# Optimization experiments

Hardware: AMD Instinct MI355X
Metric: run time of the kernel (lower is better)

## Reference

```python
import jax, jax.numpy as jnp
import numpy as np

B, S, H, NH = 2, 2048, 1024, 16
HD = H // NH

def setup_inputs() -> dict:
    key = jax.random.key(0)
    ks = jax.random.split(key, 10)
    f = lambda k, shape, scale: jax.random.normal(k, shape, dtype=jnp.float32) * scale
    return {
        "hidden_states": f(ks[0], (B, S, H), 1.0),
        "attention_mask": f(ks[1], (B, 1, S, S), 1.0),
        # static weights: randn * static_ratio(0.9); dynamic: randn * 0.01
        "q_static": f(ks[2], (H, H), 0.9), "q_dynamic": f(ks[3], (H, H), 0.01),
        "k_static": f(ks[4], (H, H), 0.9), "k_dynamic": f(ks[5], (H, H), 0.01),
        "v_static": f(ks[6], (H, H), 0.9), "v_dynamic": f(ks[7], (H, H), 0.01),
        "o_static": f(ks[8], (H, H), 0.9), "o_dynamic": f(ks[9], (H, H), 0.01),
    }

def _split_heads(x):
    # [B, S, H] -> [B, NH, S, HD]
    b, s, _ = x.shape
    return x.reshape(b, s, NH, HD).transpose(0, 2, 1, 3)

def reference(hidden_states, attention_mask,
              q_static, q_dynamic, k_static, k_dynamic,
              v_static, v_dynamic, o_static, o_dynamic):
    # DualWeightLinear: y = x @ (static + dynamic)^T  (no bias)
    q = hidden_states @ (q_static + q_dynamic).T
    k = hidden_states @ (k_static + k_dynamic).T
    v = hidden_states @ (v_static + v_dynamic).T
    q, k, v = _split_heads(q), _split_heads(k), _split_heads(v)  # [B,NH,S,HD]
    scale = 1.0 / np.sqrt(HD).astype(np.float32)
    scores = jnp.einsum('bhqd,bhkd->bhqk', q, k) * scale  # [B,NH,S,S]
    scores = scores + attention_mask  # additive mask, broadcast over heads
    attn = jax.nn.softmax(scores, axis=-1)
    out = jnp.einsum('bhqk,bhkd->bhqd', attn, v)
    out = out.transpose(0, 2, 1, 3).reshape(hidden_states.shape[0], hidden_states.shape[1], H)
    return out @ (o_static + o_dynamic).T
```

## Files before the change

### kernel.cpp

```cpp
#include <hip/hip_runtime.h>
#include <hip/hip_bf16.h>
#include <stdint.h>

#define BB 2
#define SS 2048
#define HH 1024
#define NHH 16
#define HDD 64
#define MM (BB*SS)

typedef __attribute__((ext_vector_type(8))) short short8;
typedef __attribute__((ext_vector_type(4))) float f32x4;
typedef __attribute__((ext_vector_type(4))) unsigned short u16x4;

__device__ __forceinline__ unsigned short f2bf(float x){
  unsigned u = __float_as_uint(x);
  u += 0x7fffu + ((u >> 16) & 1u);
  return (unsigned short)(u >> 16);
}
__device__ __forceinline__ float bf2f(unsigned short h){
  return __uint_as_float(((unsigned)h) << 16);
}

__global__ void k_split(const float* __restrict__ in, unsigned short* __restrict__ hi,
                        unsigned short* __restrict__ lo, int n4){
  int i = blockIdx.x * blockDim.x + threadIdx.x;
  if (i >= n4) return;
  f32x4 x = ((const f32x4*)in)[i];
  u16x4 h, l;
  #pragma unroll
  for (int j = 0; j < 4; ++j){
    unsigned short hb = f2bf(x[j]);
    h[j] = hb;
    l[j] = f2bf(x[j] - bf2f(hb));
  }
  ((u16x4*)hi)[i] = h;
  ((u16x4*)lo)[i] = l;
}

__global__ void k_addsplit(const float* __restrict__ a, const float* __restrict__ b,
                           unsigned short* __restrict__ hi, unsigned short* __restrict__ lo, int n4){
  int i = blockIdx.x * blockDim.x + threadIdx.x;
  if (i >= n4) return;
  f32x4 x = ((const f32x4*)a)[i] + ((const f32x4*)b)[i];
  u16x4 h, l;
  #pragma unroll
  for (int j = 0; j < 4; ++j){
    unsigned short hb = f2bf(x[j]);
    h[j] = hb;
    l[j] = f2bf(x[j] - bf2f(hb));
  }
  ((u16x4*)hi)[i] = h;
  ((u16x4*)lo)[i] = l;
}

__global__ void k_addplain(const float* __restrict__ a, const float* __restrict__ b,
                           unsigned short* __restrict__ w, int n4){
  int i = blockIdx.x * blockDim.x + threadIdx.x;
  if (i >= n4) return;
  f32x4 x = ((const f32x4*)a)[i] + ((const f32x4*)b)[i];
  u16x4 h;
  #pragma unroll
  for (int j = 0; j < 4; ++j) h[j] = f2bf(x[j]);
  ((u16x4*)w)[i] = h;
}

template<int EPI>
__global__ __launch_bounds__(256, 2)
void gemm_bt(const unsigned short* __restrict__ A, const unsigned short* __restrict__ Bm,
             void* __restrict__ Cout, int M, int N, int K)
{
  __shared__ unsigned short As[128*32];
  __shared__ unsigned short Bs[128*32];
  const int tid = threadIdx.x;
  const int mb0 = blockIdx.y * 128, nb0 = blockIdx.x * 128;
  const int w  = tid >> 6, lane = tid & 63;
  const int wr = w >> 1,  wc = w & 1;
  const int lg = lane >> 4, lr = lane & 15;

  f32x4 zero4 = {0.f, 0.f, 0.f, 0.f};
  f32x4 acc[4][4];
  #pragma unroll
  for (int mi = 0; mi < 4; ++mi)
    #pragma unroll
    for (int ni = 0; ni < 4; ++ni) acc[mi][ni] = zero4;

  const unsigned short* Abase = A  + (size_t)mb0 * K;
  const unsigned short* Bbase = Bm + (size_t)nb0 * K;

  for (int kb = 0; kb < K; kb += 32) {
    __syncthreads();
    #pragma unroll
    for (int i = 0; i < 2; ++i){
      int c = i*256 + tid;
      int row = c >> 2, off = (c & 3) << 3;
      size_t go = (size_t)row * K + kb + off;
      __builtin_amdgcn_global_load_lds(
          (const __attribute__((address_space(1))) void*)(Abase + go),
          (__attribute__((address_space(3))) void*)(&As[c*8]), 16, 0, 0);
      __builtin_amdgcn_global_load_lds(
          (const __attribute__((address_space(1))) void*)(Bbase + go),
          (__attribute__((address_space(3))) void*)(&Bs[c*8]), 16, 0, 0);
    }
    __syncthreads();
    short8 af[4], bfr[4];
    #pragma unroll
    for (int mi = 0; mi < 4; ++mi) af[mi]  = *(const short8*)&As[(wr*64 + mi*16 + lr)*32 + lg*8];
    #pragma unroll
    for (int ni = 0; ni < 4; ++ni) bfr[ni] = *(const short8*)&Bs[(wc*64 + ni*16 + lr)*32 + lg*8];
    #pragma unroll
    for (int mi = 0; mi < 4; ++mi)
      #pragma unroll
      for (int ni = 0; ni < 4; ++ni)
        acc[mi][ni] = __builtin_amdgcn_mfma_f32_16x16x32_bf16(af[mi], bfr[ni], acc[mi][ni], 0, 0, 0);
  }

  #pragma unroll
  for (int mi = 0; mi < 4; ++mi){
    #pragma unroll
    for (int ni = 0; ni < 4; ++ni){
      int n  = nb0 + wc*64 + ni*16 + lr;
      int m0 = mb0 + wr*64 + mi*16 + 4*lg;
      if constexpr (EPI == 1) {
        unsigned short* vt = (unsigned short*)Cout;
        int b = m0 >> 11, s0 = m0 & 2047;
        u16x4 pk;
        #pragma unroll
        for (int r = 0; r < 4; ++r) pk[r] = f2bf(acc[mi][ni][r]);
        *(u16x4*)&vt[((size_t)(b*HH + n))*SS + s0] = pk;
      } else {
        float* C = (float*)Cout;
        #pragma unroll
        for (int r = 0; r < 4; ++r) C[(size_t)(m0 + r)*N + n] = acc[mi][ni][r];
      }
    }
  }
}

__global__ __launch_bounds__(256, 2)
void gemm_bt_split(const unsigned short* __restrict__ Ah, const unsigned short* __restrict__ Al,
                   const unsigned short* __restrict__ Bh, const unsigned short* __restrict__ Bl,
                   unsigned short* __restrict__ Ch, unsigned short* __restrict__ Cl,
                   int M, int N, int K)
{
  __shared__ unsigned short Ash[128*32], Asl[128*32], Bsh[128*32], Bsl[128*32];
  const int tid = threadIdx.x;
  const int mb0 = blockIdx.y * 128, nb0 = blockIdx.x * 128;
  const int w  = tid >> 6, lane = tid & 63;
  const int wr = w >> 1,  wc = w & 1;
  const int lg = lane >> 4, lr = lane & 15;

  f32x4 zero4 = {0.f, 0.f, 0.f, 0.f};
  f32x4 acc[4][4];
  #pragma unroll
  for (int mi = 0; mi < 4; ++mi)
    #pragma unroll
    for (int ni = 0; ni < 4; ++ni) acc[mi][ni] = zero4;

  const unsigned short* Ahb = Ah + (size_t)mb0 * K;
  const unsigned short* Alb = Al + (size_t)mb0 * K;
  const unsigned short* Bhb = Bh + (size_t)nb0 * K;
  const unsigned short* Blb = Bl + (size_t)nb0 * K;

  for (int kb = 0; kb < K; kb += 32) {
    __syncthreads();
    #pragma unroll
    for (int i = 0; i < 2; ++i){
      int c = i*256 + tid;
      int row = c >> 2, off = (c & 3) << 3;
      size_t go = (size_t)row * K + kb + off;
      __builtin_amdgcn_global_load_lds(
          (const __attribute__((address_space(1))) void*)(Ahb + go),
          (__attribute__((address_space(3))) void*)(&Ash[c*8]), 16, 0, 0);
      __builtin_amdgcn_global_load_lds(
          (const __attribute__((address_space(1))) void*)(Alb + go),
          (__attribute__((address_space(3))) void*)(&Asl[c*8]), 16, 0, 0);
      __builtin_amdgcn_global_load_lds(
          (const __attribute__((address_space(1))) void*)(Bhb + go),
          (__attribute__((address_space(3))) void*)(&Bsh[c*8]), 16, 0, 0);
      __builtin_amdgcn_global_load_lds(
          (const __attribute__((address_space(1))) void*)(Blb + go),
          (__attribute__((address_space(3))) void*)(&Bsl[c*8]), 16, 0, 0);
    }
    __syncthreads();
    short8 ah4[4], al4[4], bh4[4], bl4[4];
    #pragma unroll
    for (int mi = 0; mi < 4; ++mi){
      int ro = (wr*64 + mi*16 + lr)*32 + lg*8;
      ah4[mi] = *(const short8*)&Ash[ro];
      al4[mi] = *(const short8*)&Asl[ro];
    }
    #pragma unroll
    for (int ni = 0; ni < 4; ++ni){
      int ro = (wc*64 + ni*16 + lr)*32 + lg*8;
      bh4[ni] = *(const short8*)&Bsh[ro];
      bl4[ni] = *(const short8*)&Bsl[ro];
    }
    #pragma unroll
    for (int mi = 0; mi < 4; ++mi)
      #pragma unroll
      for (int ni = 0; ni < 4; ++ni){
        acc[mi][ni] = __builtin_amdgcn_mfma_f32_16x16x32_bf16(ah4[mi], bh4[ni], acc[mi][ni], 0, 0, 0);
        acc[mi][ni] = __builtin_amdgcn_mfma_f32_16x16x32_bf16(al4[mi], bh4[ni], acc[mi][ni], 0, 0, 0);
        acc[mi][ni] = __builtin_amdgcn_mfma_f32_16x16x32_bf16(ah4[mi], bl4[ni], acc[mi][ni], 0, 0, 0);
      }
  }

  #pragma unroll
  for (int mi = 0; mi < 4; ++mi){
    #pragma unroll
    for (int ni = 0; ni < 4; ++ni){
      int n  = nb0 + wc*64 + ni*16 + lr;
      int m0 = mb0 + wr*64 + mi*16 + 4*lg;
      #pragma unroll
      for (int r = 0; r < 4; ++r){
        float x = acc[mi][ni][r];
        unsigned short hb = f2bf(x);
        unsigned short lb = f2bf(x - bf2f(hb));
        size_t o = (size_t)(m0 + r)*N + n;
        Ch[o] = hb;
        Cl[o] = lb;
      }
    }
  }
}

__global__ __launch_bounds__(512, 4)
void attn_fwd(const unsigned short* __restrict__ qh, const unsigned short* __restrict__ ql,
              const unsigned short* __restrict__ kh, const unsigned short* __restrict__ kl,
              const unsigned short* __restrict__ vt, const float* __restrict__ mask,
              unsigned short* __restrict__ ao)
{
  __shared__ unsigned short Ksh[2][64*64];
  __shared__ unsigned short Ksl[2][64*64];
  __shared__ unsigned short Vss[2][64*64];
  __shared__ unsigned short P[8][16*64];

  const int tid = threadIdx.x;
  const int w = tid >> 6, lane = tid & 63;
  const int lg = lane >> 4, lr = lane & 15;
  const int xork = (lr & 7) << 4;

  const int bid = (blockIdx.x & 7) * 64 + (blockIdx.x >> 3);
  const int qb = bid & 15, h = (bid >> 4) & 15, b = bid >> 8;
  const int q0 = qb*128 + w*16;
  const int hoff = h*64;

  const int srow = tid >> 3;
  const int sgx  = (tid & 7) ^ (srow & 7);

  short8 qfh[2], qfl[2];
  {
    size_t qoff = ((size_t)(b*SS + q0 + lr))*HH + hoff + lg*8;
    qfh[0] = *(const short8*)(qh + qoff);
    qfl[0] = *(const short8*)(ql + qoff);
    qfh[1] = *(const short8*)(qh + qoff + 32);
    qfl[1] = *(const short8*)(ql + qoff + 32);
  }

  float m_run[4] = {-1e30f, -1e30f, -1e30f, -1e30f};
  float l_run[4] = {0.f, 0.f, 0.f, 0.f};
  f32x4 zero4 = {0.f, 0.f, 0.f, 0.f};
  f32x4 acc[4];
  #pragma unroll
  for (int d4 = 0; d4 < 4; ++d4) acc[d4] = zero4;
  const size_t mrow = ((size_t)(b*SS + q0 + 4*lg))*SS;

  #define ATTN_STAGE(buf, kvb) do {                                              \
    size_t kro = ((size_t)(b*SS + (kvb) + srow))*HH + hoff + sgx*8;              \
    size_t vro = ((size_t)(b*HH + hoff + srow))*SS + (kvb) + sgx*8;              \
    __builtin_amdgcn_global_load_lds(                                            \
        (const __attribute__((address_space(1))) void*)(kh + kro),               \
        (__attribute__((address_space(3))) void*)(&Ksh[buf][tid*8]), 16, 0, 0);  \
    __builtin_amdgcn_global_load_lds(                                            \
        (const __attribute__((address_space(1))) void*)(kl + kro),               \
        (__attribute__((address_space(3))) void*)(&Ksl[buf][tid*8]), 16, 0, 0);  \
    __builtin_amdgcn_global_load_lds(                                            \
        (const __attribute__((address_space(1))) void*)(vt + vro),               \
        (__attribute__((address_space(3))) void*)(&Vss[buf][tid*8]), 16, 0, 0);  \
  } while (0)

  ATTN_STAGE(0, 0);

  for (int t = 0; t < SS/64; ++t) {
    const int kv = t*64;
    const int cur = t & 1;
    __syncthreads();
    if (t + 1 < SS/64) ATTN_STAGE(cur ^ 1, kv + 64);

    float mk[4][4];
    #pragma unroll
    for (int r = 0; r < 4; ++r)
      #pragma unroll
      for (int nb = 0; nb < 4; ++nb)
        mk[r][nb] = mask[mrow + (size_t)r*SS + kv + nb*16 + lr];

    f32x4 sc[4];
    #pragma unroll
    for (int nb = 0; nb < 4; ++nb) {
      const int krow = (nb*16 + lr)*64;
      const int c0 = ((0   + lg*16) ^ xork) >> 1;
      const int c1 = ((64  + lg*16) ^ xork) >> 1;
      short8 k0h = *(const short8*)&Ksh[cur][krow + c0];
      short8 k1h = *(const short8*)&Ksh[cur][krow + c1];
      short8 k0l = *(const short8*)&Ksl[cur][krow + c0];
      short8 k1l = *(const short8*)&Ksl[cur][krow + c1];
      f32x4 d = zero4;
      d = __builtin_amdgcn_mfma_f32_16x16x32_bf16(qfh[0], k0h, d, 0, 0, 0);
      d = __builtin_amdgcn_mfma_f32_16x16x32_bf16(qfh[1], k1h, d, 0, 0, 0);
      d = __builtin_amdgcn_mfma_f32_16x16x32_bf16(qfh[0], k0l, d, 0, 0, 0);
      d = __builtin_amdgcn_mfma_f32_16x16x32_bf16(qfh[1], k1l, d, 0, 0, 0);
      d = __builtin_amdgcn_mfma_f32_16x16x32_bf16(qfl[0], k0h, d, 0, 0, 0);
      d = __builtin_amdgcn_mfma_f32_16x16x32_bf16(qfl[1], k1h, d, 0, 0, 0);
      sc[nb] = d;
    }

    float s[4][4], rmax[4];
    #pragma unroll
    for (int r = 0; r < 4; ++r) {
      float a0 = fmaf(sc[0][r], 0.125f, mk[r][0]);
      float a1 = fmaf(sc[1][r], 0.125f, mk[r][1]);
      float a2 = fmaf(sc[2][r], 0.125f, mk[r][2]);
      float a3 = fmaf(sc[3][r], 0.125f, mk[r][3]);
      s[0][r] = a0; s[1][r] = a1; s[2][r] = a2; s[3][r] = a3;
      rmax[r] = fmaxf(fmaxf(a0, a1), fmaxf(a2, a3));
    }
    #pragma unroll
    for (int off = 1; off < 16; off <<= 1) {
      #pragma unroll
      for (int r = 0; r < 4; ++r) rmax[r] = fmaxf(rmax[r], __shfl_xor(rmax[r], off, 16));
    }
    float corr[4];
    #pragma unroll
    for (int r = 0; r < 4; ++r) {
      float mn = fmaxf(m_run[r], rmax[r]);
      corr[r] = __expf(m_run[r] - mn);
      m_run[r] = mn;
      const int prow = 4*lg + r;
      const int pxor = (prow & 7) << 4;
      float lsum = 0.f;
      #pragma unroll
      for (int nb = 0; nb < 4; ++nb) {
        float pv = __expf(s[nb][r] - mn);
        unsigned short pb = f2bf(pv);
        lsum += bf2f(pb);
        P[w][prow*64 + (((((nb*16 + lr) << 1)) ^ pxor) >> 1)] = pb;
      }
      l_run[r] = l_run[r]*corr[r] + lsum;
    }
    #pragma unroll
    for (int d4 = 0; d4 < 4; ++d4)
      #pragma unroll
      for (int r = 0; r < 4; ++r) acc[d4][r] *= corr[r];

    const int p0 = ((0  + lg*16) ^ xork) >> 1;
    const int p1 = ((64 + lg*16) ^ xork) >> 1;
    short8 pf0 = *(const short8*)&P[w][lr*64 + p0];
    short8 pf1 = *(const short8*)&P[w][lr*64 + p1];
    #pragma unroll
    for (int d4 = 0; d4 < 4; ++d4) {
      const int vrow = (d4*16 + lr)*64;
      short8 vf0 = *(const short8*)&Vss[cur][vrow + p0];
      short8 vf1 = *(const short8*)&Vss[cur][vrow + p1];
      acc[d4] = __builtin_amdgcn_mfma_f32_16x16x32_bf16(pf0, vf0, acc[d4], 0, 0, 0);
      acc[d4] = __builtin_amdgcn_mfma_f32_16x16x32_bf16(pf1, vf1, acc[d4], 0, 0, 0);
    }
  }
  #undef ATTN_STAGE

  #pragma unroll
  for (int off = 1; off < 16; off <<= 1) {
    #pragma unroll
    for (int r = 0; r < 4; ++r) l_run[r] += __shfl_xor(l_run[r], off, 16);
  }
  #pragma unroll
  for (int r = 0; r < 4; ++r) l_run[r] = 1.0f / l_run[r];
  #pragma unroll
  for (int d4 = 0; d4 < 4; ++d4)
    #pragma unroll
    for (int r = 0; r < 4; ++r) {
      size_t o = ((size_t)(b*SS + q0 + 4*lg + r))*HH + hoff + d4*16 + lr;
      ao[o] = f2bf(acc[d4][r] * l_run[r]);
    }
}

extern "C" void kernel_launch(void* const* d_in, const int* in_sizes, int n_in,
                              void* d_out, int out_size, void* d_ws, size_t ws_size,
                              hipStream_t stream)
{
  const float* hs  = (const float*)d_in[0];
  const float* msk = (const float*)d_in[1];
  const float* qs  = (const float*)d_in[2];
  const float* qd  = (const float*)d_in[3];
  const float* ks  = (const float*)d_in[4];
  const float* kd  = (const float*)d_in[5];
  const float* vs  = (const float*)d_in[6];
  const float* vd  = (const float*)d_in[7];
  const float* os_ = (const float*)d_in[8];
  const float* od  = (const float*)d_in[9];
  float* out = (float*)d_out;

  const size_t NHS = (size_t)MM * HH;
  const size_t NW  = (size_t)HH * HH;
  unsigned short* p = (unsigned short*)d_ws;
  unsigned short* hsh = p; p += NHS;
  unsigned short* hsl = p; p += NHS;
  unsigned short* wqh = p; p += NW;
  unsigned short* wql = p; p += NW;
  unsigned short* wkh = p; p += NW;
  unsigned short* wkl = p; p += NW;
  unsigned short* wv  = p; p += NW;
  unsigned short* wo  = p; p += NW;
  unsigned short* qhB = p; p += NHS;
  unsigned short* qlB = p; p += NHS;
  unsigned short* khB = p; p += NHS;
  unsigned short* klB = p; p += NHS;
  unsigned short* vtB = p; p += NHS;
  unsigned short* aoB = p; p += NHS;

  k_split  <<<(int)(NHS/1024), 256, 0, stream>>>(hs, hsh, hsl, (int)(NHS/4));
  k_addsplit<<<(int)(NW/1024), 256, 0, stream>>>(qs, qd, wqh, wql, (int)(NW/4));
  k_addsplit<<<(int)(NW/1024), 256, 0, stream>>>(ks, kd, wkh, wkl, (int)(NW/4));
  k_addplain<<<(int)(NW/1024), 256, 0, stream>>>(vs, vd, wv, (int)(NW/4));
  k_addplain<<<(int)(NW/1024), 256, 0, stream>>>(os_, od, wo, (int)(NW/4));

  dim3 gg(HH/128, MM/128);
  gemm_bt_split<<<gg, 256, 0, stream>>>(hsh, hsl, wqh, wql, qhB, qlB, MM, HH, HH);
  gemm_bt_split<<<gg, 256, 0, stream>>>(hsh, hsl, wkh, wkl, khB, klB, MM, HH, HH);
  gemm_bt<1><<<gg, 256, 0, stream>>>(hsh, wv, (void*)vtB, MM, HH, HH);

  attn_fwd<<<BB*NHH*(SS/128), 512, 0, stream>>>(qhB, qlB, khB, klB, vtB, msk, aoB);

  gemm_bt<2><<<gg, 256, 0, stream>>>(aoB, wo, (void*)out, MM, HH, HH);
}
```

Measured before the change: 365.2 us.

## Fuse weight prep and QKV projections, permute mask, compute row sums via MFMA

Merges the four weight add/split kernels into one launch and the three Q/K/V projection GEMMs into a single grid that picks its weight by column block. Adds a pre-pass that permutes the attention mask so each lane reads it with vector loads, at the cost of an extra full read and write of the mask. In attention, the softmax denominator is now accumulated with an MFMA against a ones vector instead of scalar sums and a final shuffle reduction. Some bf16 conversions switch to the library intrinsic.

```diff
diff --git a/kernel.cpp b/kernel.cpp
--- a/kernel.cpp
+++ b/kernel.cpp
@@ -8,6 +8,7 @@
 #define NHH 16
 #define HDD 64
 #define MM (BB*SS)
+#define N4SEG (HH*HH/4)
 
 typedef __attribute__((ext_vector_type(8))) short short8;
 typedef __attribute__((ext_vector_type(4))) float f32x4;
@@ -20,6 +21,10 @@
 }
 __device__ __forceinline__ float bf2f(unsigned short h){
   return __uint_as_float(((unsigned)h) << 16);
+}
+__device__ __forceinline__ unsigned short f2bf_fast(float x){
+  __hip_bfloat16 hb = __float2bfloat16(x);
+  return *reinterpret_cast<unsigned short*>(&hb);
 }
 
 __global__ void k_split(const float* __restrict__ in, unsigned short* __restrict__ hi,
@@ -38,37 +43,172 @@
   ((u16x4*)lo)[i] = l;
 }
 
-__global__ void k_addsplit(const float* __restrict__ a, const float* __restrict__ b,
-                           unsigned short* __restrict__ hi, unsigned short* __restrict__ lo, int n4){
+__global__ void k_wprep(const float* __restrict__ qs, const float* __restrict__ qd,
+                        const float* __restrict__ ks, const float* __restrict__ kd,
+                        const float* __restrict__ vs, const float* __restrict__ vd,
+                        const float* __restrict__ os_, const float* __restrict__ od,
+                        unsigned short* __restrict__ wqh, unsigned short* __restrict__ wql,
+                        unsigned short* __restrict__ wkh, unsigned short* __restrict__ wkl,
+                        unsigned short* __restrict__ wv,  unsigned short* __restrict__ wo){
   int i = blockIdx.x * blockDim.x + threadIdx.x;
-  if (i >= n4) return;
-  f32x4 x = ((const f32x4*)a)[i] + ((const f32x4*)b)[i];
+  int seg = i >> 18;
+  int j = i & (N4SEG - 1);
+  const float *pa, *pb; unsigned short *ph, *pl = nullptr;
+  if      (seg == 0){ pa = qs; pb = qd; ph = wqh; pl = wql; }
+  else if (seg == 1){ pa = ks; pb = kd; ph = wkh; pl = wkl; }
+  else if (seg == 2){ pa = vs; pb = vd; ph = wv; }
+  else              { pa = os_; pb = od; ph = wo; }
+  f32x4 x = ((const f32x4*)pa)[j] + ((const f32x4*)pb)[j];
   u16x4 h, l;
   #pragma unroll
-  for (int j = 0; j < 4; ++j){
-    unsigned short hb = f2bf(x[j]);
-    h[j] = hb;
-    l[j] = f2bf(x[j] - bf2f(hb));
-  }
-  ((u16x4*)hi)[i] = h;
-  ((u16x4*)lo)[i] = l;
-}
-
-__global__ void k_addplain(const float* __restrict__ a, const float* __restrict__ b,
-                           unsigned short* __restrict__ w, int n4){
+  for (int c = 0; c < 4; ++c){
+    unsigned short hb = f2bf(x[c]);
+    h[c] = hb;
+    l[c] = f2bf(x[c] - bf2f(hb));
+  }
+  ((u16x4*)ph)[j] = h;
+  if (pl) ((u16x4*)pl)[j] = l;
+}
+
+__global__ void k_maskperm(const float* __restrict__ m, float* __restrict__ pm){
   int i = blockIdx.x * blockDim.x + threadIdx.x;
-  if (i >= n4) return;
-  f32x4 x = ((const f32x4*)a)[i] + ((const f32x4*)b)[i];
-  u16x4 h;
-  #pragma unroll
-  for (int j = 0; j < 4; ++j) h[j] = f2bf(x[j]);
-  ((u16x4*)w)[i] = h;
-}
-
-template<int EPI>
+  int lr = i & 15;
+  int q  = (i >> 4) & 2047;
+  int t  = (i >> 15) & 31;
+  int b  = i >> 20;
+  const float* src = m + ((size_t)(b*2048 + q))*2048 + t*64 + lr;
+  f32x4 v = { src[0], src[16], src[32], src[48] };
+  ((f32x4*)pm)[i] = v;
+}
+
 __global__ __launch_bounds__(256, 2)
-void gemm_bt(const unsigned short* __restrict__ A, const unsigned short* __restrict__ Bm,
-             void* __restrict__ Cout, int M, int N, int K)
+void proj_fused(const unsigned short* __restrict__ hsh, const unsigned short* __restrict__ hsl,
+                const unsigned short* __restrict__ wqh, const unsigned short* __restrict__ wql,
+                const unsigned short* __restrict__ wkh, const unsigned short* __restrict__ wkl,
+                const unsigned short* __restrict__ wv,
+                unsigned short* __restrict__ qhB, unsigned short* __restrict__ qlB,
+                unsigned short* __restrict__ khB, unsigned short* __restrict__ klB,
+                unsigned short* __restrict__ vtB)
+{
+  __shared__ unsigned short Ash[128*32], Asl[128*32], Bsh[128*32], Bsl[128*32];
+  const int tid = threadIdx.x;
+  const int nb0 = blockIdx.x * 128;
+  const int mb0 = blockIdx.y * 128;
+  const int kind = nb0 >> 10;
+  const int ncol0 = nb0 & 1023;
+  const int w  = tid >> 6, lane = tid & 63;
+  const int wr = w >> 1,  wc = w & 1;
+  const int lg = lane >> 4, lr = lane & 15;
+
+  const unsigned short* Bh = (kind == 0 ? wqh : (kind == 1 ? wkh : wv)) + (size_t)ncol0 * HH;
+  const unsigned short* Bl = (kind == 0 ? wql : wkl) + (size_t)ncol0 * HH;
+  const unsigned short* Ahb = hsh + (size_t)mb0 * HH;
+  const unsigned short* Alb = hsl + (size_t)mb0 * HH;
+
+  f32x4 zero4 = {0.f, 0.f, 0.f, 0.f};
+  f32x4 acc[4][4];
+  #pragma unroll
+  for (int mi = 0; mi < 4; ++mi)
+    #pragma unroll
+    for (int ni = 0; ni < 4; ++ni) acc[mi][ni] = zero4;
+
+  for (int kb = 0; kb < HH; kb += 32) {
+    __syncthreads();
+    #pragma unroll
+    for (int i = 0; i < 2; ++i){
+      int c = i*256 + tid;
+      int row = c >> 2, off = (c & 3) << 3;
+      size_t go = (size_t)row * HH + kb + off;
+      __builtin_amdgcn_global_load_lds(
+          (const __attribute__((address_space(1))) void*)(Ahb + go),
+          (__attribute__((address_space(3))) void*)(&Ash[c*8]), 16, 0, 0);
+      __builtin_amdgcn_global_load_lds(
+          (const __attribute__((address_space(1))) void*)(Alb + go),
+          (__attribute__((address_space(3))) void*)(&Asl[c*8]), 16, 0, 0);
+      __builtin_amdgcn_global_load_lds(
+          (const __attribute__((address_space(1))) void*)(Bh + go),
+          (__attribute__((address_space(3))) void*)(&Bsh[c*8]), 16, 0, 0);
+      if (kind < 2)
+        __builtin_amdgcn_global_load_lds(
+            (const __attribute__((address_space(1))) void*)(Bl + go),
+            (__attribute__((address_space(3))) void*)(&Bsl[c*8]), 16, 0, 0);
+    }
+    __syncthreads();
+    short8 ah4[4], al4[4], bh4[4], bl4[4];
+    #pragma unroll
+    for (int mi = 0; mi < 4; ++mi){
+      int ro = (wr*64 + mi*16 + lr)*32 + lg*8;
+      ah4[mi] = *(const short8*)&Ash[ro];
+      al4[mi] = *(const short8*)&Asl[ro];
+    }
+    #pragma unroll
+    for (int ni = 0; ni < 4; ++ni){
+      int ro = (wc*64 + ni*16 + lr)*32 + lg*8;
+      bh4[ni] = *(const short8*)&Bsh[ro];
+    }
+    if (kind < 2) {
+      #pragma unroll
+      for (int ni = 0; ni < 4; ++ni){
+        int ro = (wc*64 + ni*16 + lr)*32 + lg*8;
+        bl4[ni] = *(const short8*)&Bsl[ro];
+      }
+      #pragma unroll
+      for (int mi = 0; mi < 4; ++mi)
+        #pragma unroll
+        for (int ni = 0; ni < 4; ++ni){
+          acc[mi][ni] = __builtin_amdgcn_mfma_f32_16x16x32_bf16(ah4[mi], bh4[ni], acc[mi][ni], 0, 0, 0);
+          acc[mi][ni] = __builtin_amdgcn_mfma_f32_16x16x32_bf16(al4[mi], bh4[ni], acc[mi][ni], 0, 0, 0);
+          acc[mi][ni] = __builtin_amdgcn_mfma_f32_16x16x32_bf16(ah4[mi], bl4[ni], acc[mi][ni], 0, 0, 0);
+        }
+    } else {
+      #pragma unroll
+      for (int mi = 0; mi < 4; ++mi)
+        #pragma unroll
+        for (int ni = 0; ni < 4; ++ni)
+          acc[mi][ni] = __builtin_amdgcn_mfma_f32_16x16x32_bf16(ah4[mi], bh4[ni], acc[mi][ni], 0, 0, 0);
+    }
+  }
+
+  if (kind == 2) {
+    #pragma unroll
+    for (int mi = 0; mi < 4; ++mi){
+      #pragma unroll
+      for (int ni = 0; ni < 4; ++ni){
+        int nv = ncol0 + wc*64 + ni*16 + lr;
+        int m0 = mb0 + wr*64 + mi*16 + 4*lg;
+        int b = m0 >> 11, s0 = m0 & 2047;
+        u16x4 pk;
+        #pragma unroll
+        for (int r = 0; r < 4; ++r) pk[r] = f2bf_fast(acc[mi][ni][r]);
+        *(u16x4*)&vtB[((size_t)(b*HH + nv))*SS + s0] = pk;
+      }
+    }
+  } else {
+    unsigned short* Ch = (kind == 0) ? qhB : khB;
+    unsigned short* Cl = (kind == 0) ? qlB : klB;
+    #pragma unroll
+    for (int mi = 0; mi < 4; ++mi){
+      #pragma unroll
+      for (int ni = 0; ni < 4; ++ni){
+        int n  = ncol0 + wc*64 + ni*16 + lr;
+        int m0 = mb0 + wr*64 + mi*16 + 4*lg;
+        #pragma unroll
+        for (int r = 0; r < 4; ++r){
+          float x = acc[mi][ni][r];
+          unsigned short hb = f2bf(x);
+          unsigned short lb = f2bf(x - bf2f(hb));
+          size_t o = (size_t)(m0 + r)*HH + n;
+          Ch[o] = hb;
+          Cl[o] = lb;
+        }
+      }
+    }
+  }
+}
+
+__global__ __launch_bounds__(256, 2)
+void gemm_o(const unsigned short* __restrict__ A, const unsigned short* __restrict__ Bm,
+            float* __restrict__ C, int M, int N, int K)
 {
   __shared__ unsigned short As[128*32];
   __shared__ unsigned short Bs[128*32];
@@ -121,106 +261,8 @@
     for (int ni = 0; ni < 4; ++ni){
       int n  = nb0 + wc*64 + ni*16 + lr;
       int m0 = mb0 + wr*64 + mi*16 + 4*lg;
-      if constexpr (EPI == 1) {
-        unsigned short* vt = (unsigned short*)Cout;
-        int b = m0 >> 11, s0 = m0 & 2047;
-        u16x4 pk;
-        #pragma unroll
-        for (int r = 0; r < 4; ++r) pk[r] = f2bf(acc[mi][ni][r]);
-        *(u16x4*)&vt[((size_t)(b*HH + n))*SS + s0] = pk;
-      } else {
-        float* C = (float*)Cout;
-        #pragma unroll
-        for (int r = 0; r < 4; ++r) C[(size_t)(m0 + r)*N + n] = acc[mi][ni][r];
-      }
-    }
-  }
-}
-
-__global__ __launch_bounds__(256, 2)
-void gemm_bt_split(const unsigned short* __restrict__ Ah, const unsigned short* __restrict__ Al,
-                   const unsigned short* __restrict__ Bh, const unsigned short* __restrict__ Bl,
-                   unsigned short* __restrict__ Ch, unsigned short* __restrict__ Cl,
-                   int M, int N, int K)
-{
-  __shared__ unsigned short Ash[128*32], Asl[128*32], Bsh[128*32], Bsl[128*32];
-  const int tid = threadIdx.x;
-  const int mb0 = blockIdx.y * 128, nb0 = blockIdx.x * 128;
-  const int w  = tid >> 6, lane = tid & 63;
-  const int wr = w >> 1,  wc = w & 1;
-  const int lg = lane >> 4, lr = lane & 15;
-
-  f32x4 zero4 = {0.f, 0.f, 0.f, 0.f};
-  f32x4 acc[4][4];
-  #pragma unroll
-  for (int mi = 0; mi < 4; ++mi)
-    #pragma unroll
-    for (int ni = 0; ni < 4; ++ni) acc[mi][ni] = zero4;
-
-  const unsigned short* Ahb = Ah + (size_t)mb0 * K;
-  const unsigned short* Alb = Al + (size_t)mb0 * K;
-  const unsigned short* Bhb = Bh + (size_t)nb0 * K;
-  const unsigned short* Blb = Bl + (size_t)nb0 * K;
-
-  for (int kb = 0; kb < K; kb += 32) {
-    __syncthreads();
-    #pragma unroll
-    for (int i = 0; i < 2; ++i){
-      int c = i*256 + tid;
-      int row = c >> 2, off = (c & 3) << 3;
-      size_t go = (size_t)row * K + kb + off;
-      __builtin_amdgcn_global_load_lds(
-          (const __attribute__((address_space(1))) void*)(Ahb + go),
-          (__attribute__((address_space(3))) void*)(&Ash[c*8]), 16, 0, 0);
-      __builtin_amdgcn_global_load_lds(
-          (const __attribute__((address_space(1))) void*)(Alb + go),
-          (__attribute__((address_space(3))) void*)(&Asl[c*8]), 16, 0, 0);
-      __builtin_amdgcn_global_load_lds(
-          (const __attribute__((address_space(1))) void*)(Bhb + go),
-          (__attribute__((address_space(3))) void*)(&Bsh[c*8]), 16, 0, 0);
-      __builtin_amdgcn_global_load_lds(
-          (const __attribute__((address_space(1))) void*)(Blb + go),
-          (__attribute__((address_space(3))) void*)(&Bsl[c*8]), 16, 0, 0);
-    }
-    __syncthreads();
-    short8 ah4[4], al4[4], bh4[4], bl4[4];
-    #pragma unroll
-    for (int mi = 0; mi < 4; ++mi){
-      int ro = (wr*64 + mi*16 + lr)*32 + lg*8;
-      ah4[mi] = *(const short8*)&Ash[ro];
-      al4[mi] = *(const short8*)&Asl[ro];
-    }
-    #pragma unroll
-    for (int ni = 0; ni < 4; ++ni){
-      int ro = (wc*64 + ni*16 + lr)*32 + lg*8;
-      bh4[ni] = *(const short8*)&Bsh[ro];
-      bl4[ni] = *(const short8*)&Bsl[ro];
-    }
-    #pragma unroll
-    for (int mi = 0; mi < 4; ++mi)
-      #pragma unroll
-      for (int ni = 0; ni < 4; ++ni){
-        acc[mi][ni] = __builtin_amdgcn_mfma_f32_16x16x32_bf16(ah4[mi], bh4[ni], acc[mi][ni], 0, 0, 0);
-        acc[mi][ni] = __builtin_amdgcn_mfma_f32_16x16x32_bf16(al4[mi], bh4[ni], acc[mi][ni], 0, 0, 0);
-        acc[mi][ni] = __builtin_amdgcn_mfma_f32_16x16x32_bf16(ah4[mi], bl4[ni], acc[mi][ni], 0, 0, 0);
-      }
-  }
-
-  #pragma unroll
-  for (int mi = 0; mi < 4; ++mi){
-    #pragma unroll
-    for (int ni = 0; ni < 4; ++ni){
-      int n  = nb0 + wc*64 + ni*16 + lr;
-      int m0 = mb0 + wr*64 + mi*16 + 4*lg;
-      #pragma unroll
-      for (int r = 0; r < 4; ++r){
-        float x = acc[mi][ni][r];
-        unsigned short hb = f2bf(x);
-        unsigned short lb = f2bf(x - bf2f(hb));
-        size_t o = (size_t)(m0 + r)*N + n;
-        Ch[o] = hb;
-        Cl[o] = lb;
-      }
+      #pragma unroll
+      for (int r = 0; r < 4; ++r) C[(size_t)(m0 + r)*N + n] = acc[mi][ni][r];
     }
   }
 }
@@ -228,7 +270,7 @@
 __global__ __launch_bounds__(512, 4)
 void attn_fwd(const unsigned short* __restrict__ qh, const unsigned short* __restrict__ ql,
               const unsigned short* __restrict__ kh, const unsigned short* __restrict__ kl,
-              const unsigned short* __restrict__ vt, const float* __restrict__ mask,
+              const unsigned short* __restrict__ vt, const float* __restrict__ pm,
               unsigned short* __restrict__ ao)
 {
   __shared__ unsigned short Ksh[2][64*64];
@@ -257,14 +299,17 @@
     qfh[1] = *(const short8*)(qh + qoff + 32);
     qfl[1] = *(const short8*)(ql + qoff + 32);
   }
+  short8 ones8;
+  #pragma unroll
+  for (int j = 0; j < 8; ++j) ones8[j] = (short)0x3F80;
 
   float m_run[4] = {-1e30f, -1e30f, -1e30f, -1e30f};
-  float l_run[4] = {0.f, 0.f, 0.f, 0.f};
   f32x4 zero4 = {0.f, 0.f, 0.f, 0.f};
-  f32x4 acc[4];
+  f32x4 acc[4], acc_l = zero4;
   #pragma unroll
   for (int d4 = 0; d4 < 4; ++d4) acc[d4] = zero4;
-  const size_t mrow = ((size_t)(b*SS + q0 + 4*lg))*SS;
+
+  const float* mbase = pm + ((size_t)b*32*2048 + q0 + 4*lg)*64 + (size_t)lr*4;
 
   #define ATTN_STAGE(buf, kvb) do {                                              \
     size_t kro = ((size_t)(b*SS + (kvb) + srow))*HH + hoff + sgx*8;              \
@@ -288,19 +333,17 @@
     __syncthreads();
     if (t + 1 < SS/64) ATTN_STAGE(cur ^ 1, kv + 64);
 
-    float mk[4][4];
-    #pragma unroll
-    for (int r = 0; r < 4; ++r)
-      #pragma unroll
-      for (int nb = 0; nb < 4; ++nb)
-        mk[r][nb] = mask[mrow + (size_t)r*SS + kv + nb*16 + lr];
+    const float* mp = mbase + (size_t)t*(2048*64);
+    f32x4 mk4[4];
+    #pragma unroll
+    for (int r = 0; r < 4; ++r) mk4[r] = *(const f32x4*)(mp + r*64);
 
     f32x4 sc[4];
+    const int c0 = ((0  + lg*16) ^ xork) >> 1;
+    const int c1 = ((64 + lg*16) ^ xork) >> 1;
     #pragma unroll
     for (int nb = 0; nb < 4; ++nb) {
       const int krow = (nb*16 + lr)*64;
-      const int c0 = ((0   + lg*16) ^ xork) >> 1;
-      const int c1 = ((64  + lg*16) ^ xork) >> 1;
       short8 k0h = *(const short8*)&Ksh[cur][krow + c0];
       short8 k1h = *(const short8*)&Ksh[cur][krow + c1];
       short8 k0l = *(const short8*)&Ksl[cur][krow + c0];
@@ -318,10 +361,10 @@
     float s[4][4], rmax[4];
     #pragma unroll
     for (int r = 0; r < 4; ++r) {
-      float a0 = fmaf(sc[0][r], 0.125f, mk[r][0]);
-      float a1 = fmaf(sc[1][r], 0.125f, mk[r][1]);
-      float a2 = fmaf(sc[2][r], 0.125f, mk[r][2]);
-      float a3 = fmaf(sc[3][r], 0.125f, mk[r][3]);
+      float a0 = fmaf(sc[0][r], 0.125f, mk4[r][0]);
+      float a1 = fmaf(sc[1][r], 0.125f, mk4[r][1]);
+      float a2 = fmaf(sc[2][r], 0.125f, mk4[r][2]);
+      float a3 = fmaf(sc[3][r], 0.125f, mk4[r][3]);
       s[0][r] = a0; s[1][r] = a1; s[2][r] = a2; s[3][r] = a3;
       rmax[r] = fmaxf(fmaxf(a0, a1), fmaxf(a2, a3));
     }
@@ -338,25 +381,24 @@
       m_run[r] = mn;
       const int prow = 4*lg + r;
       const int pxor = (prow & 7) << 4;
-      float lsum = 0.f;
       #pragma unroll
       for (int nb = 0; nb < 4; ++nb) {
         float pv = __expf(s[nb][r] - mn);
-        unsigned short pb = f2bf(pv);
-        lsum += bf2f(pb);
-        P[w][prow*64 + (((((nb*16 + lr) << 1)) ^ pxor) >> 1)] = pb;
+        P[w][prow*64 + (((((nb*16 + lr) << 1)) ^ pxor) >> 1)] = f2bf_fast(pv);
       }
-      l_run[r] = l_run[r]*corr[r] + lsum;
     }
     #pragma unroll
     for (int d4 = 0; d4 < 4; ++d4)
       #pragma unroll
       for (int r = 0; r < 4; ++r) acc[d4][r] *= corr[r];
-
-    const int p0 = ((0  + lg*16) ^ xork) >> 1;
-    const int p1 = ((64 + lg*16) ^ xork) >> 1;
+    #pragma unroll
+    for (int r = 0; r < 4; ++r) acc_l[r] *= corr[r];
+
+    const int p0 = c0, p1 = c1;
     short8 pf0 = *(const short8*)&P[w][lr*64 + p0];
     short8 pf1 = *(const short8*)&P[w][lr*64 + p1];
+    acc_l = __builtin_amdgcn_mfma_f32_16x16x32_bf16(pf0, ones8, acc_l, 0, 0, 0);
+    acc_l = __builtin_amdgcn_mfma_f32_16x16x32_bf16(pf1, ones8, acc_l, 0, 0, 0);
     #pragma unroll
     for (int d4 = 0; d4 < 4; ++d4) {
       const int vrow = (d4*16 + lr)*64;
@@ -368,19 +410,15 @@
   }
   #undef ATTN_STAGE
 
-  #pragma unroll
-  for (int off = 1; off < 16; off <<= 1) {
-    #pragma unroll
-    for (int r = 0; r < 4; ++r) l_run[r] += __shfl_xor(l_run[r], off, 16);
-  }
-  #pragma unroll
-  for (int r = 0; r < 4; ++r) l_run[r] = 1.0f / l_run[r];
+  float inv[4];
+  #pragma unroll
+  for (int r = 0; r < 4; ++r) inv[r] = 1.0f / acc_l[r];
   #pragma unroll
   for (int d4 = 0; d4 < 4; ++d4)
     #pragma unroll
     for (int r = 0; r < 4; ++r) {
       size_t o = ((size_t)(b*SS + q0 + 4*lg + r))*HH + hoff + d4*16 + lr;
-      ao[o] = f2bf(acc[d4][r] * l_run[r]);
+      ao[o] = f2bf_fast(acc[d4][r] * inv[r]);
     }
 }
 
@@ -417,19 +455,17 @@
   unsigned short* klB = p; p += NHS;
   unsigned short* vtB = p; p += NHS;
   unsigned short* aoB = p; p += NHS;
-
-  k_split  <<<(int)(NHS/1024), 256, 0, stream>>>(hs, hsh, hsl, (int)(NHS/4));
-  k_addsplit<<<(int)(NW/1024), 256, 0, stream>>>(qs, qd, wqh, wql, (int)(NW/4));
-  k_addsplit<<<(int)(NW/1024), 256, 0, stream>>>(ks, kd, wkh, wkl, (int)(NW/4));
-  k_addplain<<<(int)(NW/1024), 256, 0, stream>>>(vs, vd, wv, (int)(NW/4));
-  k_addplain<<<(int)(NW/1024), 256, 0, stream>>>(os_, od, wo, (int)(NW/4));
-
-  dim3 gg(HH/128, MM/128);
-  gemm_bt_split<<<gg, 256, 0, stream>>>(hsh, hsl, wqh, wql, qhB, qlB, MM, HH, HH);
-  gemm_bt_split<<<gg, 256, 0, stream>>>(hsh, hsl, wkh, wkl, khB, klB, MM, HH, HH);
-  gemm_bt<1><<<gg, 256, 0, stream>>>(hsh, wv, (void*)vtB, MM, HH, HH);
-
-  attn_fwd<<<BB*NHH*(SS/128), 512, 0, stream>>>(qhB, qlB, khB, klB, vtB, msk, aoB);
-
-  gemm_bt<2><<<gg, 256, 0, stream>>>(aoB, wo, (void*)out, MM, HH, HH);
-}
+  float* pm = (float*)p;
+
+  k_split   <<<(int)(NHS/1024), 256, 0, stream>>>(hs, hsh, hsl, (int)(NHS/4));
+  k_wprep   <<<(int)(4*N4SEG/256), 256, 0, stream>>>(qs, qd, ks, kd, vs, vd, os_, od,
+                                                     wqh, wql, wkh, wkl, wv, wo);
+  k_maskperm<<<8192, 256, 0, stream>>>(msk, pm);
+
+  proj_fused<<<dim3(3*HH/128, MM/128), 256, 0, stream>>>(hsh, hsl, wqh, wql, wkh, wkl, wv,
+                                                         qhB, qlB, khB, klB, vtB);
+
+  attn_fwd<<<BB*NHH*(SS/128), 512, 0, stream>>>(qhB, qlB, khB, klB, vtB, pm, aoB);
+
+  gemm_o<<<dim3(HH/128, MM/128), 256, 0, stream>>>(aoB, wo, out, MM, HH, HH);
+}
```

After: 353.7 us. -3.1%, faster.
